# Kernel optimization log

Measured on AMD Instinct MI355X. Metric: run time of the kernel, lower is better.

The kernel has to match this reference:

```python
import jax, jax.numpy as jnp
import numpy as np

N_NODES = 100000


def gcn_conv(x, W, b, src, dst, n):
    """PyG GCNConv: add self-loops, symmetric normalization, aggregate."""
    x = x @ W  # [N, out]
    loop = jnp.arange(n, dtype=src.dtype)
    src_f = jnp.concatenate([src, loop])  # sources (message origins)
    dst_f = jnp.concatenate([dst, loop])  # targets (aggregation index)
    ones = jnp.ones(src_f.shape[0], dtype=x.dtype)
    deg = jax.ops.segment_sum(ones, dst_f, num_segments=n)
    dinv = jnp.where(deg > 0, jax.lax.rsqrt(deg), 0.0)
    norm = dinv[src_f] * dinv[dst_f]  # [E+N]
    msg = x[src_f] * norm[:, None]  # gather + scale
    out = jax.ops.segment_sum(msg, dst_f, num_segments=n)  # scatter-add
    return out + b


def setup_inputs() -> dict:
    key = jax.random.key(0)
    k1, k2, k3, k4 = jax.random.split(key, 4)
    in_f, hid, ncls = 128, 128, 64
    n_edges = 1600000
    x = jax.random.normal(k1, (N_NODES, in_f), dtype=jnp.float32)
    W1 = jax.random.normal(k2, (in_f, hid), dtype=jnp.float32) * (1.0 / np.sqrt(in_f))
    b1 = jnp.zeros((hid,), dtype=jnp.float32)
    W2 = jax.random.normal(k3, (hid, ncls), dtype=jnp.float32) * (1.0 / np.sqrt(hid))
    b2 = jnp.zeros((ncls,), dtype=jnp.float32)
    edge_index = jax.random.randint(k4, (2, n_edges), 0, N_NODES, dtype=jnp.int32)
    return {"x": x, "W1": W1, "b1": b1, "W2": W2, "b2": b2, "edge_index": edge_index}


def reference(x, W1, b1, W2, b2, edge_index):
    src, dst = edge_index[0], edge_index[1]
    n = x.shape[0]
    h = gcn_conv(x, W1, b1, src, dst, n)
    h = jax.nn.relu(h)
    # dropout p=0.5 is identity in eval mode
    h = gcn_conv(h, W2, b2, src, dst, n)
    return jax.nn.log_softmax(h, axis=1)
```

## Files before the change

kernel.cpp:

```cpp
#include <hip/hip_runtime.h>
#include <math.h>

#define N_NODES 100000
#define N_EDGES 1600000
#define NB 391
#define MROWS 100096
#define CH 3200

typedef __attribute__((ext_vector_type(8))) short short8;
typedef __attribute__((ext_vector_type(4))) float f32x4;
typedef __attribute__((ext_vector_type(2))) float f32x2;

__device__ __forceinline__ short f2b(float f) {
    unsigned u = __float_as_uint(f);
    unsigned r = (u + 0x7FFFu + ((u >> 16) & 1u)) >> 16;
    return (short)r;
}
__device__ __forceinline__ unsigned pk2(float a, float b) {
    return (unsigned)(unsigned short)f2b(a) | ((unsigned)(unsigned short)f2b(b) << 16);
}
__device__ __forceinline__ unsigned char f2q(float v) {
    return (unsigned char)(__builtin_amdgcn_cvt_pk_fp8_f32(v, 0.f, 0, false) & 0xFF);
}
__device__ __forceinline__ void acc2(f32x2* a, unsigned u) {
    a[0] += __builtin_amdgcn_cvt_pk_f32_fp8((int)u, false);
    a[1] += __builtin_amdgcn_cvt_pk_f32_fp8((int)u, true);
}
__device__ __forceinline__ void acc16(f32x2* a, uint4 u) {
    acc2(a + 0, u.x); acc2(a + 2, u.y); acc2(a + 4, u.z); acc2(a + 6, u.w);
}

__device__ __forceinline__ short8 pack8t(const float* __restrict__ p) {
    float4 v0 = ((const float4*)p)[0];
    float4 v1 = ((const float4*)p)[1];
    union { unsigned u[4]; short8 s; } r;
    r.u[0] = __builtin_amdgcn_perm(__float_as_uint(v0.y), __float_as_uint(v0.x), 0x07060302u);
    r.u[1] = __builtin_amdgcn_perm(__float_as_uint(v0.w), __float_as_uint(v0.z), 0x07060302u);
    r.u[2] = __builtin_amdgcn_perm(__float_as_uint(v1.y), __float_as_uint(v1.x), 0x07060302u);
    r.u[3] = __builtin_amdgcn_perm(__float_as_uint(v1.w), __float_as_uint(v1.z), 0x07060302u);
    return r.s;
}

__global__ __launch_bounds__(512) void init_misc(int* __restrict__ bcnt) {
    int t = threadIdx.x;
    if (t < NB) bcnt[t] = 0;
}

__global__ __launch_bounds__(256) void bucket_count(const int* __restrict__ dst,
                                                    int* __restrict__ bcnt) {
    __shared__ int h[NB];
    int t = threadIdx.x;
    for (int i = t; i < NB; i += 256) h[i] = 0;
    __syncthreads();
    for (int e = blockIdx.x * 256 + t; e < N_EDGES; e += gridDim.x * 256)
        atomicAdd(&h[dst[e] >> 8], 1);
    __syncthreads();
    for (int i = t; i < NB; i += 256)
        if (h[i]) atomicAdd(&bcnt[i], h[i]);
}

__global__ __launch_bounds__(512) void bucket_scan(const int* __restrict__ bcnt,
                                                   int* __restrict__ boffs,
                                                   int* __restrict__ bcur) {
    __shared__ int s[512];
    int t = threadIdx.x;
    int v = (t < NB) ? bcnt[t] : 0;
    s[t] = v;
    __syncthreads();
    for (int off = 1; off < 512; off <<= 1) {
        int u = (t >= off) ? s[t - off] : 0;
        __syncthreads();
        s[t] += u;
        __syncthreads();
    }
    if (t < NB) {
        int ex = s[t] - v;
        boffs[t] = ex;
        bcur[t] = ex;
    }
    if (t == 0) boffs[NB] = N_EDGES;
}

__global__ __launch_bounds__(256) void bucket_scatter(const int* __restrict__ src,
                                                      const int* __restrict__ dst,
                                                      int* __restrict__ bcur,
                                                      unsigned* __restrict__ pairs) {
    __shared__ unsigned lw[CH];
    __shared__ short lb[CH];
    __shared__ int cnt[NB];
    __shared__ int lstart[NB];
    int t = threadIdx.x;
    int e0 = blockIdx.x * CH;
    int n = min(CH, N_EDGES - e0);
    for (int i = t; i < NB; i += 256) cnt[i] = 0;
    __syncthreads();
    for (int i = t; i < n; i += 256) {
        int s = src[e0 + i], d = dst[e0 + i];
        lw[i] = ((unsigned)(d & 255) << 24) | (unsigned)s;
        int b = d >> 8;
        lb[i] = (short)b;
        atomicAdd(&cnt[b], 1);
    }
    __syncthreads();
    for (int b = t; b < NB; b += 256) {
        int c = cnt[b];
        lstart[b] = c ? atomicAdd(&bcur[b], c) : 0;
        cnt[b] = 0;
    }
    __syncthreads();
    for (int i = t; i < n; i += 256) {
        int b = lb[i];
        int lo = atomicAdd(&cnt[b], 1);
        pairs[lstart[b] + lo] = lw[i];
    }
}

__global__ __launch_bounds__(256) void csr_fill_bucket(const unsigned* __restrict__ pairs,
                                                       const int* __restrict__ boffs,
                                                       int2* __restrict__ rinfo,
                                                       float* __restrict__ dinv,
                                                       int* __restrict__ srcs) {
    __shared__ int lcnt[256];
    __shared__ int ls[256];
    int t = threadIdx.x, b = blockIdx.x, base = b << 8;
    lcnt[t] = 0;
    __syncthreads();
    int lo_e = boffs[b], hi_e = boffs[b + 1];
    for (int i = lo_e + t; i < hi_e; i += 256)
        atomicAdd(&lcnt[pairs[i] >> 24], 1);
    __syncthreads();
    int c = lcnt[t];
    int len = c + 1;
    ls[t] = len;
    __syncthreads();
    for (int off = 1; off < 256; off <<= 1) {
        int u = (t >= off) ? ls[t - off] : 0;
        __syncthreads();
        ls[t] += u;
        __syncthreads();
    }
    int rp = lo_e + base + ls[t] - len;
    int node = base + t;
    if (node < N_NODES) {
        rinfo[node] = make_int2(rp, rp + len);
        dinv[node] = rsqrtf((float)len);
        srcs[rp] = node;
    }
    __syncthreads();
    lcnt[t] = rp + 1;
    __syncthreads();
    for (int i = lo_e + t; i < hi_e; i += 256) {
        unsigned p = pairs[i];
        int li = p >> 24;
        int pos = atomicAdd(&lcnt[li], 1);
        srcs[pos] = (int)(p & 0xFFFFFFu);
    }
}

__global__ __launch_bounds__(256) void convert_w(const float* __restrict__ W1,
                                                 const float* __restrict__ W2,
                                                 short* __restrict__ w1h,
                                                 short* __restrict__ w2h) {
    int id = blockIdx.x * 256 + threadIdx.x;
    if (id < 128 * 128) {
        int n = id >> 7, k = id & 127;
        w1h[id] = f2b(W1[k * 128 + n]);
    } else if (id < 128 * 128 + 64 * 128) {
        int j = id - 128 * 128;
        int n = j >> 7, k = j & 127;
        w2h[j] = f2b(W2[k * 64 + n]);
    }
}

__global__ __launch_bounds__(512) void gemm1_mfma(const float* __restrict__ X,
                                                  const short* __restrict__ Wt,
                                                  const float* __restrict__ dinv,
                                                  unsigned char* __restrict__ Yf) {
    __shared__ short Ws[128 * 128];
    const int t = threadIdx.x;
    for (int i = t * 8; i < 128 * 128; i += 512 * 8)
        *(short8*)(Ws + i) = *(const short8*)(Wt + i);
    __syncthreads();

    const int w = t >> 6, lane = t & 63;
    const int m = lane & 15, q = lane >> 4;
    const int r0 = blockIdx.x * 128 + w * 16;
    const int ra = min(r0 + m, N_NODES - 1);

    f32x4 acc[8];
#pragma unroll
    for (int c = 0; c < 8; ++c) acc[c] = (f32x4)(0.f);

#pragma unroll
    for (int kk = 0; kk < 4; ++kk) {
        const int koff = kk * 32 + q * 8;
        short8 a = pack8t(X + (size_t)ra * 128 + koff);
#pragma unroll
        for (int c = 0; c < 8; ++c) {
            short8 bh = *(const short8*)(Ws + (c * 16 + m) * 128 + koff);
            acc[c] = __builtin_amdgcn_mfma_f32_16x16x32_bf16(a, bh, acc[c], 0, 0, 0);
        }
    }

    const int rb0 = r0 + q * 4;
    f32x4 dv = *(const f32x4*)(dinv + rb0);
#pragma unroll
    for (int c = 0; c < 8; ++c) {
        const int col = c * 16 + m;
#pragma unroll
        for (int r = 0; r < 4; ++r) {
            int row = rb0 + r;
            if (row < N_NODES) Yf[(size_t)row * 128 + col] = f2q(acc[c][r] * dv[r]);
        }
    }
}

__global__ __launch_bounds__(512) void gemm2_mfma(const short* __restrict__ H,
                                                  const short* __restrict__ Wt,
                                                  const float* __restrict__ dinv,
                                                  unsigned char* __restrict__ Yf) {
    __shared__ short Ws[64 * 128];
    const int t = threadIdx.x;
    for (int i = t * 8; i < 64 * 128; i += 512 * 8)
        *(short8*)(Ws + i) = *(const short8*)(Wt + i);
    __syncthreads();

    const int w = t >> 6, lane = t & 63;
    const int m = lane & 15, q = lane >> 4;
    const int r0 = blockIdx.x * 128 + w * 16;

    f32x4 acc[4];
#pragma unroll
    for (int c = 0; c < 4; ++c) acc[c] = (f32x4)(0.f);

#pragma unroll
    for (int kk = 0; kk < 4; ++kk) {
        const int koff = kk * 32 + q * 8;
        short8 a = *(const short8*)(H + (size_t)(r0 + m) * 128 + koff);
#pragma unroll
        for (int c = 0; c < 4; ++c) {
            short8 bh = *(const short8*)(Ws + (c * 16 + m) * 128 + koff);
            acc[c] = __builtin_amdgcn_mfma_f32_16x16x32_bf16(a, bh, acc[c], 0, 0, 0);
        }
    }

    const int rb0 = r0 + q * 4;
    f32x4 dv = *(const f32x4*)(dinv + rb0);
#pragma unroll
    for (int c = 0; c < 4; ++c) {
        const int col = c * 16 + m;
#pragma unroll
        for (int r = 0; r < 4; ++r) {
            int row = rb0 + r;
            if (row < N_NODES) Yf[(size_t)row * 64 + col] = f2q(acc[c][r] * dv[r]);
        }
    }
}

__global__ __launch_bounds__(256) void agg_relu(const int2* __restrict__ rinfo,
                                                const int* __restrict__ srcs,
                                                const unsigned char* __restrict__ Yf,
                                                const float* __restrict__ dinv,
                                                const float* __restrict__ b,
                                                short* __restrict__ Hb) {
    int t = threadIdx.x;
    int lane = t & 63, w = t >> 6;
    int g = lane >> 3, fl = lane & 7;
    int node = blockIdx.x * 32 + w * 8 + g;
    const unsigned fo = (unsigned)(fl << 4);
    int2 r = rinfo[node];
    int e = r.x, len = r.y - r.x;
    int mx = len;
    mx = max(mx, __shfl_xor(mx, 8));
    mx = max(mx, __shfl_xor(mx, 16));
    mx = max(mx, __shfl_xor(mx, 32));
    f32x2 a[8];
#pragma unroll
    for (int i = 0; i < 8; ++i) a[i] = (f32x2)(0.f);

    uint4 GA0, GA1;
    unsigned sB0 = 0, sB1 = 0;
    {
        unsigned s0 = (unsigned)srcs[e];
        GA0 = *(const uint4*)(Yf + ((s0 << 7) + fo));
        if (1 < len) {
            unsigned s1 = (unsigned)srcs[e + 1];
            GA1 = *(const uint4*)(Yf + ((s1 << 7) + fo));
        }
        if (2 < len) sB0 = (unsigned)srcs[e + 2];
        if (3 < len) sB1 = (unsigned)srcs[e + 3];
    }
    for (int i = 0; i < mx; i += 2) {
        uint4 GB0, GB1;
        if (i + 2 < len) GB0 = *(const uint4*)(Yf + ((sB0 << 7) + fo));
        if (i + 3 < len) GB1 = *(const uint4*)(Yf + ((sB1 << 7) + fo));
        unsigned sC0 = sB0, sC1 = sB1;
        if (i + 4 < len) sC0 = (unsigned)srcs[e + i + 4];
        if (i + 5 < len) sC1 = (unsigned)srcs[e + i + 5];
        if (i < len)     acc16(a, GA0);
        if (i + 1 < len) acc16(a, GA1);
        GA0 = GB0; GA1 = GB1; sB0 = sC0; sB1 = sC1;
    }

    float sc = dinv[node];
    const float4* bf = (const float4*)b;
    float bb[16];
    *(float4*)(bb + 0)  = bf[fl * 4 + 0];
    *(float4*)(bb + 4)  = bf[fl * 4 + 1];
    *(float4*)(bb + 8)  = bf[fl * 4 + 2];
    *(float4*)(bb + 12) = bf[fl * 4 + 3];
    unsigned u[8];
#pragma unroll
    for (int k = 0; k < 8; ++k) {
        float v0 = fmaxf(sc * a[k][0] + bb[2 * k], 0.f);
        float v1 = fmaxf(sc * a[k][1] + bb[2 * k + 1], 0.f);
        u[k] = pk2(v0, v1);
    }
    uint4* hp = (uint4*)Hb + (size_t)node * 16 + fl * 2;
    hp[0] = make_uint4(u[0], u[1], u[2], u[3]);
    hp[1] = make_uint4(u[4], u[5], u[6], u[7]);
}

__global__ __launch_bounds__(256) void agg_lsm(const int2* __restrict__ rinfo,
                                               const int* __restrict__ srcs,
                                               const unsigned char* __restrict__ Yf,
                                               const float* __restrict__ dinv,
                                               const float* __restrict__ b,
                                               float* __restrict__ out) {
    int t = threadIdx.x;
    int lane = t & 63, w = t >> 6;
    int g = lane >> 2, fl = lane & 3;
    int node = blockIdx.x * 64 + w * 16 + g;
    int nd = min(node, N_NODES - 1);
    const unsigned fo = (unsigned)(fl << 4);
    int2 r = rinfo[nd];
    int e = r.x, len = r.y - r.x;
    int mx = len;
    mx = max(mx, __shfl_xor(mx, 4));
    mx = max(mx, __shfl_xor(mx, 8));
    mx = max(mx, __shfl_xor(mx, 16));
    mx = max(mx, __shfl_xor(mx, 32));
    f32x2 a[8];
#pragma unroll
    for (int i = 0; i < 8; ++i) a[i] = (f32x2)(0.f);

    uint4 GA0, GA1;
    unsigned sB0 = 0, sB1 = 0;
    {
        unsigned s0 = (unsigned)srcs[e];
        GA0 = *(const uint4*)(Yf + ((s0 << 6) + fo));
        if (1 < len) {
            unsigned s1 = (unsigned)srcs[e + 1];
            GA1 = *(const uint4*)(Yf + ((s1 << 6) + fo));
        }
        if (2 < len) sB0 = (unsigned)srcs[e + 2];
        if (3 < len) sB1 = (unsigned)srcs[e + 3];
    }
    for (int i = 0; i < mx; i += 2) {
        uint4 GB0, GB1;
        if (i + 2 < len) GB0 = *(const uint4*)(Yf + ((sB0 << 6) + fo));
        if (i + 3 < len) GB1 = *(const uint4*)(Yf + ((sB1 << 6) + fo));
        unsigned sC0 = sB0, sC1 = sB1;
        if (i + 4 < len) sC0 = (unsigned)srcs[e + i + 4];
        if (i + 5 < len) sC1 = (unsigned)srcs[e + i + 5];
        if (i < len)     acc16(a, GA0);
        if (i + 1 < len) acc16(a, GA1);
        GA0 = GB0; GA1 = GB1; sB0 = sC0; sB1 = sC1;
    }

    float sc = dinv[nd];
    const float4* bf = (const float4*)b;
    float bb[16];
    *(float4*)(bb + 0)  = bf[fl * 4 + 0];
    *(float4*)(bb + 4)  = bf[fl * 4 + 1];
    *(float4*)(bb + 8)  = bf[fl * 4 + 2];
    *(float4*)(bb + 12) = bf[fl * 4 + 3];
    float v[16];
#pragma unroll
    for (int j = 0; j < 16; ++j) v[j] = sc * a[j >> 1][j & 1] + bb[j];
    float m = v[0];
#pragma unroll
    for (int j = 1; j < 16; ++j) m = fmaxf(m, v[j]);
    m = fmaxf(m, __shfl_xor(m, 1));
    m = fmaxf(m, __shfl_xor(m, 2));
    float su = 0.f;
#pragma unroll
    for (int j = 0; j < 16; ++j) su += __expf(v[j] - m);
    su += __shfl_xor(su, 1);
    su += __shfl_xor(su, 2);
    float ls = m + logf(su);
    if (node < N_NODES) {
        float4* op = (float4*)out + (size_t)node * 16 + fl * 4;
        op[0] = make_float4(v[0] - ls,  v[1] - ls,  v[2] - ls,  v[3] - ls);
        op[1] = make_float4(v[4] - ls,  v[5] - ls,  v[6] - ls,  v[7] - ls);
        op[2] = make_float4(v[8] - ls,  v[9] - ls,  v[10] - ls, v[11] - ls);
        op[3] = make_float4(v[12] - ls, v[13] - ls, v[14] - ls, v[15] - ls);
    }
}

extern "C" void kernel_launch(void* const* d_in, const int* in_sizes, int n_in,
                              void* d_out, int out_size, void* d_ws, size_t ws_size,
                              hipStream_t stream) {
    const float* x  = (const float*)d_in[0];
    const float* W1 = (const float*)d_in[1];
    const float* b1 = (const float*)d_in[2];
    const float* W2 = (const float*)d_in[3];
    const float* b2 = (const float*)d_in[4];
    const int* edge = (const int*)d_in[5];
    const int* src = edge;
    const int* dst = edge + N_EDGES;
    float* out = (float*)d_out;

    char* ws = (char*)d_ws;
    int*           bcnt  = (int*)(ws + 0);
    int*           boffs = (int*)(ws + 2048);
    int*           bcur  = (int*)(ws + 4096);
    float*         dinv  = (float*)(ws + 6144);
    int2*          rinfo = (int2*)(ws + 406528);
    int*           srcs  = (int*)(ws + 1206528);
    unsigned*      pairs = (unsigned*)(ws + 14012672);
    short*         w1h   = (short*)(ws + 20412672);
    short*         w2h   = (short*)(ws + 20445440);
    unsigned char* y1f   = (unsigned char*)(ws + 20461824);
    short*         h1b   = (short*)(ws + 33274112);
    unsigned char* y2f   = (unsigned char*)(ws + 58898688);

    init_misc<<<1, 512, 0, stream>>>(bcnt);

    bucket_count<<<512, 256, 0, stream>>>(dst, bcnt);
    bucket_scan<<<1, 512, 0, stream>>>(bcnt, boffs, bcur);
    bucket_scatter<<<(N_EDGES + CH - 1) / CH, 256, 0, stream>>>(src, dst, bcur, pairs);
    csr_fill_bucket<<<NB, 256, 0, stream>>>(pairs, boffs, rinfo, dinv, srcs);

    convert_w<<<(128 * 128 + 64 * 128 + 255) / 256, 256, 0, stream>>>(W1, W2, w1h, w2h);

    gemm1_mfma<<<MROWS / 128, 512, 0, stream>>>(x, w1h, dinv, y1f);
    agg_relu<<<N_NODES / 32, 256, 0, stream>>>(rinfo, srcs, y1f, dinv, b1, h1b);

    gemm2_mfma<<<MROWS / 128, 512, 0, stream>>>(h1b, w2h, dinv, y2f);
    agg_lsm<<<(N_NODES + 63) / 64, 256, 0, stream>>>(rinfo, srcs, y2f, dinv, b2, out);
}
```

Before: 257.9 us.

## Stage bucket scatter writes in LDS and deepen gather prefetch in agg_relu

```diff
diff --git a/kernel.cpp b/kernel.cpp
--- a/kernel.cpp
+++ b/kernel.cpp
@@ -81,38 +81,55 @@
     if (t == 0) boffs[NB] = N_EDGES;
 }
 
-__global__ __launch_bounds__(256) void bucket_scatter(const int* __restrict__ src,
+__global__ __launch_bounds__(512) void bucket_scatter(const int* __restrict__ src,
                                                       const int* __restrict__ dst,
                                                       int* __restrict__ bcur,
                                                       unsigned* __restrict__ pairs) {
     __shared__ unsigned lw[CH];
+    __shared__ unsigned lw2[CH];
+    __shared__ int gdst[CH];
     __shared__ short lb[CH];
+    __shared__ int s[512];
     __shared__ int cnt[NB];
     __shared__ int lstart[NB];
     int t = threadIdx.x;
     int e0 = blockIdx.x * CH;
     int n = min(CH, N_EDGES - e0);
-    for (int i = t; i < NB; i += 256) cnt[i] = 0;
-    __syncthreads();
-    for (int i = t; i < n; i += 256) {
-        int s = src[e0 + i], d = dst[e0 + i];
-        lw[i] = ((unsigned)(d & 255) << 24) | (unsigned)s;
+    for (int i = t; i < NB; i += 512) cnt[i] = 0;
+    __syncthreads();
+    for (int i = t; i < n; i += 512) {
+        int sv = src[e0 + i], d = dst[e0 + i];
+        lw[i] = ((unsigned)(d & 255) << 24) | (unsigned)sv;
         int b = d >> 8;
         lb[i] = (short)b;
         atomicAdd(&cnt[b], 1);
     }
     __syncthreads();
-    for (int b = t; b < NB; b += 256) {
-        int c = cnt[b];
-        lstart[b] = c ? atomicAdd(&bcur[b], c) : 0;
-        cnt[b] = 0;
-    }
-    __syncthreads();
-    for (int i = t; i < n; i += 256) {
+    int v = (t < NB) ? cnt[t] : 0;
+    s[t] = v;
+    __syncthreads();
+    for (int off = 1; off < 512; off <<= 1) {
+        int u = (t >= off) ? s[t - off] : 0;
+        __syncthreads();
+        s[t] += u;
+        __syncthreads();
+    }
+    if (t < NB) {
+        s[t] -= v;
+        lstart[t] = v ? atomicAdd(&bcur[t], v) : 0;
+        cnt[t] = 0;
+    }
+    __syncthreads();
+    for (int i = t; i < n; i += 512) {
         int b = lb[i];
-        int lo = atomicAdd(&cnt[b], 1);
-        pairs[lstart[b] + lo] = lw[i];
-    }
+        int r = atomicAdd(&cnt[b], 1);
+        int sl = s[b] + r;
+        lw2[sl] = lw[i];
+        gdst[sl] = lstart[b] + r;
+    }
+    __syncthreads();
+    for (int j = t; j < n; j += 512)
+        pairs[gdst[j]] = lw2[j];
 }
 
 __global__ __launch_bounds__(256) void csr_fill_bucket(const unsigned* __restrict__ pairs,
@@ -278,28 +295,41 @@
 #pragma unroll
     for (int i = 0; i < 8; ++i) a[i] = (f32x2)(0.f);
 
-    uint4 GA0, GA1;
-    unsigned sB0 = 0, sB1 = 0;
-    {
-        unsigned s0 = (unsigned)srcs[e];
-        GA0 = *(const uint4*)(Yf + ((s0 << 7) + fo));
-        if (1 < len) {
-            unsigned s1 = (unsigned)srcs[e + 1];
-            GA1 = *(const uint4*)(Yf + ((s1 << 7) + fo));
-        }
-        if (2 < len) sB0 = (unsigned)srcs[e + 2];
-        if (3 < len) sB1 = (unsigned)srcs[e + 3];
-    }
-    for (int i = 0; i < mx; i += 2) {
-        uint4 GB0, GB1;
-        if (i + 2 < len) GB0 = *(const uint4*)(Yf + ((sB0 << 7) + fo));
-        if (i + 3 < len) GB1 = *(const uint4*)(Yf + ((sB1 << 7) + fo));
-        unsigned sC0 = sB0, sC1 = sB1;
-        if (i + 4 < len) sC0 = (unsigned)srcs[e + i + 4];
-        if (i + 5 < len) sC1 = (unsigned)srcs[e + i + 5];
-        if (i < len)     acc16(a, GA0);
-        if (i + 1 < len) acc16(a, GA1);
-        GA0 = GB0; GA1 = GB1; sB0 = sC0; sB1 = sC1;
+    auto ld = [&](int i) -> unsigned {
+        unsigned v = 0;
+        if (i < len) v = (unsigned)srcs[e + i];
+        return v;
+    };
+    auto gth = [&](unsigned s) -> uint4 {
+        return *(const uint4*)(Yf + ((s << 7) + fo));
+    };
+
+    unsigned sA0 = ld(0), sA1 = ld(1), sB0 = ld(2), sB1 = ld(3), sC0 = ld(4), sC1 = ld(5);
+    uint4 GA0, GA1, GB0, GB1, GC0, GC1;
+    if (0 < len) GA0 = gth(sA0);
+    if (1 < len) GA1 = gth(sA1);
+    if (2 < len) GB0 = gth(sB0);
+    if (3 < len) GB1 = gth(sB1);
+    if (4 < len) GC0 = gth(sC0);
+    if (5 < len) GC1 = gth(sC1);
+    sA0 = ld(6); sA1 = ld(7); sB0 = ld(8); sB1 = ld(9); sC0 = ld(10); sC1 = ld(11);
+
+    for (int i = 0; i < mx; i += 6) {
+        if (i < len)      acc16(a, GA0);
+        if (i + 1 < len)  acc16(a, GA1);
+        if (i + 6 < len)  GA0 = gth(sA0);
+        if (i + 7 < len)  GA1 = gth(sA1);
+        if (i + 2 < len)  acc16(a, GB0);
+        if (i + 3 < len)  acc16(a, GB1);
+        if (i + 8 < len)  GB0 = gth(sB0);
+        if (i + 9 < len)  GB1 = gth(sB1);
+        if (i + 4 < len)  acc16(a, GC0);
+        if (i + 5 < len)  acc16(a, GC1);
+        if (i + 10 < len) GC0 = gth(sC0);
+        if (i + 11 < len) GC1 = gth(sC1);
+        sA0 = ld(i + 12); sA1 = ld(i + 13);
+        sB0 = ld(i + 14); sB1 = ld(i + 15);
+        sC0 = ld(i + 16); sC1 = ld(i + 17);
     }
 
     float sc = dinv[node];
@@ -429,7 +459,7 @@
 
     bucket_count<<<512, 256, 0, stream>>>(dst, bcnt);
     bucket_scan<<<1, 512, 0, stream>>>(bcnt, boffs, bcur);
-    bucket_scatter<<<(N_EDGES + CH - 1) / CH, 256, 0, stream>>>(src, dst, bcur, pairs);
+    bucket_scatter<<<(N_EDGES + CH - 1) / CH, 512, 0, stream>>>(src, dst, bcur, pairs);
     csr_fill_bucket<<<NB, 256, 0, stream>>>(pairs, boffs, rinfo, dinv, srcs);
 
     convert_w<<<(128 * 128 + 64 * 128 + 255) / 256, 256, 0, stream>>>(W1, W2, w1h, w2h);
```

After: 257.7 us. Within noise of the previous version (-0.0%).
